# Kernel tuning notes

Measured on AMD Instinct MI355X. Metric: run time of the kernel, lower is better.

Reference implementation:

```python
import jax, jax.numpy as jnp
import numpy as np

B, S, HIDDEN, NH = 2, 2048, 1024, 16
D = HIDDEN // NH  # 64
PHYS_W, CONS_W = 0.2, 0.15
LN_EPS = 1e-5


def _layernorm(x, gamma, beta):
    mu = jnp.mean(x, axis=-1, keepdims=True)
    var = jnp.mean(jnp.square(x - mu), axis=-1, keepdims=True)
    return (x - mu) * jax.lax.rsqrt(var + LN_EPS) * gamma + beta


def setup_inputs() -> dict:
    key = jax.random.key(0)
    ks = jax.random.split(key, 12)
    s = 0.02
    return {
        "cnn_features": jax.random.normal(ks[0], (B, S, HIDDEN), jnp.float32),
        "llm_features": jax.random.normal(ks[1], (B, S, HIDDEN), jnp.float32),
        # Linear weights stored [in, out] so y = x @ W + b (torch's W.T)
        "Wq": jax.random.normal(ks[2], (HIDDEN, HIDDEN), jnp.float32) * s,
        "bq": jnp.zeros((HIDDEN,), jnp.float32),
        "Wk": jax.random.normal(ks[3], (HIDDEN, HIDDEN), jnp.float32) * s,
        "bk": jnp.zeros((HIDDEN,), jnp.float32),
        "Wv": jax.random.normal(ks[4], (HIDDEN, HIDDEN), jnp.float32) * s,
        "bv": jnp.zeros((HIDDEN,), jnp.float32),
        "Wo": jax.random.normal(ks[5], (HIDDEN, HIDDEN), jnp.float32) * s,
        "bo": jnp.zeros((HIDDEN,), jnp.float32),
        "energy_emb": jax.random.normal(ks[6], (1, 1, HIDDEN), jnp.float32),
        "mass_emb": jax.random.normal(ks[7], (1, 1, HIDDEN), jnp.float32),
        "momentum_emb": jax.random.normal(ks[8], (1, 1, HIDDEN), jnp.float32),
        "gamma": jnp.ones((HIDDEN,), jnp.float32),
        "beta": jnp.zeros((HIDDEN,), jnp.float32),
    }


def reference(cnn_features, llm_features, Wq, bq, Wk, bk, Wv, bv, Wo, bo,
              energy_emb, mass_emb, momentum_emb, gamma, beta):
    Bsz, Sc, _ = cnn_features.shape
    Sl = llm_features.shape[1]

    def attn(q_in, kv_in):
        Sq, Sk = q_in.shape[1], kv_in.shape[1]
        Q = (q_in @ Wq + bq).reshape(Bsz, Sq, NH, D).transpose(0, 2, 1, 3)   # bhqd
        K = (kv_in @ Wk + bk).reshape(Bsz, Sk, NH, D).transpose(0, 2, 1, 3)  # bhkd
        V = (kv_in @ Wv + bv).reshape(Bsz, Sk, NH, D).transpose(0, 2, 1, 3)  # bhkd
        scores = jnp.einsum('bhqd,bhkd->bhqk', Q, K) / np.float32(np.sqrt(D))
        # physics biases: require Sq == Sk (elementwise Q*K), shape [B,H,Sq,1]
        energy_bias = jnp.sum(Q * K, axis=-1, keepdims=True) * PHYS_W
        mass_bias = jnp.mean(Q + K, axis=-1, keepdims=True) * CONS_W
        attn_w = jax.nn.softmax(scores + energy_bias + mass_bias, axis=-1)
        attended = jnp.einsum('bhqk,bhkd->bhqd', attn_w, V)
        attended = attended.transpose(0, 2, 1, 3).reshape(Bsz, Sq, HIDDEN)
        out = attended @ Wo + bo
        return _layernorm(q_in + out, gamma, beta)

    phys = jnp.concatenate([
        jnp.broadcast_to(energy_emb, (Bsz, 1, HIDDEN)),
        jnp.broadcast_to(mass_emb, (Bsz, 1, HIDDEN)),
        jnp.broadcast_to(momentum_emb, (Bsz, 1, HIDDEN)),
    ], axis=1)  # [B, 3, HIDDEN]
    aug_cnn = jnp.concatenate([cnn_features, phys], axis=1)  # [B, Sc+3, H]
    aug_llm = jnp.concatenate([llm_features, phys], axis=1)  # [B, Sl+3, H]

    cnn_att = attn(aug_cnn, aug_llm)
    llm_att = attn(aug_llm, aug_cnn)
    return cnn_att[:, :Sc, :], llm_att[:, :Sl, :]
```

## Files before the change

### kernel.cpp

```cpp
#include <hip/hip_runtime.h>

#define BN 2
#define SS 2048
#define SA 2051
#define HID 1024
#define NHD 16
#define DH 64
#define GSTR 32
#define VTLD 8320
#define KSTR 72
#define VSTR 40
#define MFMA16 __builtin_amdgcn_mfma_f32_16x16x32_bf16
#define QSCALE 0.18033688011112042f

typedef __attribute__((ext_vector_type(4))) float floatx4;
typedef __attribute__((ext_vector_type(8))) short bf16x8;
typedef __attribute__((ext_vector_type(2))) unsigned uintx2;

__device__ __forceinline__ float bf2f(short s) {
  union { unsigned u; float f; } v; v.u = ((unsigned)(unsigned short)s) << 16; return v.f;
}
__device__ __forceinline__ short f2bf(float f) {
  union { float f; unsigned u; } v; v.f = f;
  unsigned u = v.u;
  u += 0x7FFF + ((u >> 16) & 1);
  return (short)(u >> 16);
}
__device__ __forceinline__ unsigned pack2(float lo, float hi) {
  unsigned ul = __float_as_uint(lo) + 0x8000u;
  unsigned uh = __float_as_uint(hi) + 0x8000u;
  return __builtin_amdgcn_perm(uh, ul, 0x07060302u);
}
__device__ __forceinline__ unsigned cvtpk(float lo, float hi) {
  unsigned r;
  asm("v_cvt_pk_bf16_f32 %0, %1, %2" : "=v"(r) : "v"(lo), "v"(hi));
  return r;
}
__device__ __forceinline__ float exp2fast(float x) {
#if __has_builtin(__builtin_amdgcn_exp2f)
  return __builtin_amdgcn_exp2f(x);
#else
  float r; asm("v_exp_f32 %0, %1" : "=v"(r) : "v"(x)); return r;
#endif
}
__device__ __forceinline__ uintx2 qtrans(unsigned A, unsigned B) {
  auto t = __builtin_amdgcn_permlane32_swap(A, B, false, false);
  auto u = __builtin_amdgcn_permlane16_swap(t[0], t[1], false, false);
  uintx2 r; r[0] = u[0]; r[1] = u[1];
  return r;
}
__device__ __forceinline__ void gload16(const short* g, short* l) {
  __builtin_amdgcn_global_load_lds(
      (const __attribute__((address_space(1))) void*)g,
      (__attribute__((address_space(3))) void*)l, 16, 0, 0);
}
__device__ __forceinline__ bool in_is_f32(const unsigned* graw) {
  return graw[0] == 0x3F800000u;
}

__global__ __launch_bounds__(256) void convert_in(const void* __restrict__ src, long off,
                                                  short* __restrict__ dst, int n,
                                                  const unsigned* __restrict__ graw) {
  bool f32 = in_is_f32(graw);
  int i = (blockIdx.x * 256 + threadIdx.x) * 4;
  int stride = gridDim.x * 1024;
  if (f32) {
    const float* s = (const float*)src + off;
    for (; i < n; i += stride) {
      float4 v = *(const float4*)(s + i);
      short4 o; o.x = f2bf(v.x); o.y = f2bf(v.y); o.z = f2bf(v.z); o.w = f2bf(v.w);
      *(short4*)(dst + i) = o;
    }
  } else {
    const short* s = (const short*)src + off;
    for (; i < n; i += stride)
      *(short4*)(dst + i) = *(const short4*)(s + i);
  }
}

__global__ __launch_bounds__(256) void convert_small(
    const void* s0, const void* s1, const void* s2, const void* s3,
    const void* s4, const void* s5, const void* s6, const void* s7,
    const void* s8, short* __restrict__ dst, const unsigned* __restrict__ graw) {
  bool f32 = in_is_f32(graw);
  const void* srcs[9] = {s0, s1, s2, s3, s4, s5, s6, s7, s8};
  const void* s = srcs[blockIdx.x];
  short* d = dst + (size_t)blockIdx.x * 1024;
  for (int i = threadIdx.x; i < 1024; i += 256)
    d[i] = f32 ? f2bf(((const float*)s)[i]) : ((const short*)s)[i];
}

__global__ __launch_bounds__(256) void conv_wt(const void* __restrict__ W,
    short* __restrict__ WT, const unsigned* __restrict__ graw) {
  __shared__ short tile[32][33];
  bool f32 = in_is_f32(graw);
  int n0 = blockIdx.x * 32, k0 = blockIdx.y * 32;
  int tx = threadIdx.x & 31, ty = threadIdx.x >> 5;
#pragma unroll
  for (int i = 0; i < 4; i++) {
    int k = k0 + ty + i*8;
    short v = f32 ? f2bf(((const float*)W)[(size_t)k * HID + n0 + tx])
                  : ((const short*)W)[(size_t)k * HID + n0 + tx];
    tile[ty + i*8][tx] = v;
  }
  __syncthreads();
#pragma unroll
  for (int i = 0; i < 4; i++)
    WT[(size_t)(n0 + ty + i*8) * HID + k0 + tx] = tile[tx][ty + i*8];
}

__global__ __launch_bounds__(256) void gemm_bf(
    const short* __restrict__ A, int tailA,
    const short* __restrict__ B, int tailB,
    const short* __restrict__ embB,
    const short* __restrict__ bias, int bias_row, float scale,
    short* __restrict__ out16, float* __restrict__ out32, long ldc,
    const void* __restrict__ rc0, const void* __restrict__ rc1,
    const unsigned* __restrict__ graw) {
  __shared__ __align__(16) short sA[128 * GSTR];
  __shared__ __align__(16) short sB[128 * GSTR];
  int t = threadIdx.x;
  int wave = t >> 6, lane = t & 63, l16 = lane & 15, quad = lane >> 4;
  int nwg = gridDim.x * gridDim.y;
  int bid = blockIdx.y * gridDim.x + blockIdx.x;
  int cpx = nwg >> 3;
  int swz = (bid & 7) * cpx + (bid >> 3);
  int bx = swz % gridDim.x, by = swz / gridDim.x;
  int m0 = by * 128, n0 = bx * 128;
  int msub = (wave >> 1) * 64, nsub = (wave & 1) * 64;

  const short* apr[2]; const short* bpr[2]; short* ldA[2]; short* ldB[2];
#pragma unroll
  for (int rep = 0; rep < 2; rep++) {
    int cid = rep * 256 + t;
    int row = cid >> 2, kc = (cid & 3) * 8;
    int ra = m0 + row;
    const short* ap;
    if (tailA && ra >= 8192) ap = embB + (size_t)((ra > 8194 ? 8194 : ra) - 8192) * 1024;
    else                     ap = A + (size_t)ra * HID;
    int rb = n0 + row;
    const short* bp;
    if (tailB && rb >= 8192) bp = embB + (size_t)((rb > 8194 ? 8194 : rb) - 8192) * 1024;
    else                     bp = B + (size_t)rb * HID;
    apr[rep] = ap + kc; bpr[rep] = bp + kc;
    ldA[rep] = &sA[(rep*256 + wave*64) * 8];
    ldB[rep] = &sB[(rep*256 + wave*64) * 8];
  }
#pragma unroll
  for (int rep = 0; rep < 2; rep++) {
    gload16(apr[rep], ldA[rep]);
    gload16(bpr[rep], ldB[rep]);
  }

  floatx4 acc[4][4] = {};
  for (int k0 = 0; k0 < HID; k0 += 32) {
    __syncthreads();
    bf16x8 af[4], bf_[4];
#pragma unroll
    for (int i = 0; i < 4; i++) {
      af[i]  = *(const bf16x8*)(&sA[(msub + i*16 + l16) * GSTR + quad*8]);
      bf_[i] = *(const bf16x8*)(&sB[(nsub + i*16 + l16) * GSTR + quad*8]);
    }
    __syncthreads();
    if (k0 + 32 < HID) {
#pragma unroll
      for (int rep = 0; rep < 2; rep++) {
        gload16(apr[rep] + k0 + 32, ldA[rep]);
        gload16(bpr[rep] + k0 + 32, ldB[rep]);
      }
    }
#pragma unroll
    for (int mi = 0; mi < 4; mi++)
#pragma unroll
      for (int ni = 0; ni < 4; ni++)
        acc[mi][ni] = MFMA16(af[mi], bf_[ni], acc[mi][ni], 0, 0, 0);
  }

  bool f32in = in_is_f32(graw);
#pragma unroll
  for (int mi = 0; mi < 4; mi++)
#pragma unroll
    for (int ni = 0; ni < 4; ni++) {
      int col = n0 + nsub + ni*16 + l16;
      float bcol = bias_row ? 0.f : bf2f(bias[col]);
#pragma unroll
      for (int r = 0; r < 4; r++) {
        int m = m0 + msub + mi*16 + quad*4 + r;
        float v = (acc[mi][ni][r] + (bias_row ? bf2f(bias[m]) : bcol)) * scale;
        if (out32) {
          float res;
          if (f32in) res = ((const float*)(m < 4096 ? rc0 : rc1))[(size_t)(m & 4095) * HID + col];
          else       res = bf2f(((const short*)(m < 4096 ? rc0 : rc1))[(size_t)(m & 4095) * HID + col]);
          out32[(size_t)m * HID + col] = v + res;
        } else {
          out16[(size_t)m * ldc + col] = f2bf(v);
        }
      }
    }
}

__global__ __launch_bounds__(256, 4) void flash3(
    const short* __restrict__ Qa, const short* __restrict__ Ka,
    const short* __restrict__ VTa, short* __restrict__ att) {
  __shared__ __align__(16) short sK0[32*KSTR], sK1[32*KSTR];
  __shared__ __align__(16) short sV0[64*VSTR], sV1[64*VSTR];
  int t = threadIdx.x, wave = t >> 6, lane = t & 63;
  int l16 = lane & 15, quad = lane >> 4;
  int bid = blockIdx.x;
  int swz = (bid & 7) * 128 + (bid >> 3);
  int qt  = swz & 15;
  int h   = (swz >> 4) & 15;
  int sb  = swz >> 8;
  int side = sb >> 1, b = sb & 1;
  int qrow0 = side * 4096 + b * 2048;
  int kvb = (side ^ 1) * 4096 + b * 2048;
  int q0 = qt * 128 + wave * 32;

  const short* qp0 = Qa + (size_t)(qrow0 + q0 + l16) * HID + h*DH + quad*8;
  const short* qp1 = qp0 + 16 * HID;
  bf16x8 qa0 = *(const bf16x8*)qp0, qb0 = *(const bf16x8*)(qp0 + 32);
  bf16x8 qa1 = *(const bf16x8*)qp1, qb1 = *(const bf16x8*)(qp1 + 32);

  float rs0 = 0.f, rs1 = 0.f;
  floatx4 oA[4] = {}, oB[4] = {};

  int krow = t >> 3, kc8 = (t & 7) * 8;
  int vrow = t >> 2, vc8 = (t & 3) * 8;
  const short* kgp = Ka + (size_t)(kvb + krow) * HID + h*DH + kc8;
  const short* vgp = VTa + (size_t)(h*DH + vrow) * VTLD + kvb + vc8;
  bf16x8 kreg = *(const bf16x8*)kgp;
  bf16x8 vreg = *(const bf16x8*)vgp;
  short *kw = sK0, *vw = sV0, *ka = sK1, *va = sV1;

  for (int kv0 = 0; kv0 < 2048; kv0 += 32) {
    *(bf16x8*)(kw + krow*KSTR + kc8) = kreg;
    *(bf16x8*)(vw + vrow*VSTR + vc8) = vreg;
    __syncthreads();
    kgp += 32*HID; vgp += 32;
    kreg = *(const bf16x8*)kgp;
    vreg = *(const bf16x8*)vgp;

    bf16x8 k00 = *(const bf16x8*)(kw + l16*KSTR + quad*8);
    bf16x8 k01 = *(const bf16x8*)(kw + l16*KSTR + 32 + quad*8);
    bf16x8 k10 = *(const bf16x8*)(kw + (16 + l16)*KSTR + quad*8);
    bf16x8 k11 = *(const bf16x8*)(kw + (16 + l16)*KSTR + 32 + quad*8);
    bf16x8 v0 = *(const bf16x8*)(vw + l16*VSTR + quad*8);
    bf16x8 v1 = *(const bf16x8*)(vw + (16 + l16)*VSTR + quad*8);
    bf16x8 v2 = *(const bf16x8*)(vw + (32 + l16)*VSTR + quad*8);
    bf16x8 v3 = *(const bf16x8*)(vw + (48 + l16)*VSTR + quad*8);

    floatx4 s00 = {}, s10 = {}, s01 = {}, s11 = {};
    __builtin_amdgcn_s_setprio(1);
    s00 = MFMA16(k00, qa0, s00, 0, 0, 0); s00 = MFMA16(k01, qb0, s00, 0, 0, 0);
    s10 = MFMA16(k10, qa0, s10, 0, 0, 0); s10 = MFMA16(k11, qb0, s10, 0, 0, 0);
    s01 = MFMA16(k00, qa1, s01, 0, 0, 0); s01 = MFMA16(k01, qb1, s01, 0, 0, 0);
    s11 = MFMA16(k10, qa1, s11, 0, 0, 0); s11 = MFMA16(k11, qb1, s11, 0, 0, 0);
    __builtin_amdgcn_s_setprio(0);

    floatx4 p00, p10, p01, p11;
#pragma unroll
    for (int r = 0; r < 4; r++) {
      p00[r] = exp2fast(s00[r]); p10[r] = exp2fast(s10[r]);
      p01[r] = exp2fast(s01[r]); p11[r] = exp2fast(s11[r]);
    }
    rs0 += ((p00[0]+p00[1])+(p00[2]+p00[3])) + ((p10[0]+p10[1])+(p10[2]+p10[3]));
    rs1 += ((p01[0]+p01[1])+(p01[2]+p01[3])) + ((p11[0]+p11[1])+(p11[2]+p11[3]));

    unsigned pc00 = cvtpk(p00[0], p00[1]), pc01 = cvtpk(p00[2], p00[3]);
    unsigned pc10 = cvtpk(p10[0], p10[1]), pc11 = cvtpk(p10[2], p10[3]);
    unsigned pd00 = cvtpk(p01[0], p01[1]), pd01 = cvtpk(p01[2], p01[3]);
    unsigned pd10 = cvtpk(p11[0], p11[1]), pd11 = cvtpk(p11[2], p11[3]);
    uintx2 uA0 = qtrans(pc00, pc10);
    uintx2 uA1 = qtrans(pc01, pc11);
    uintx2 uB0 = qtrans(pd00, pd10);
    uintx2 uB1 = qtrans(pd01, pd11);
    union { unsigned u[4]; bf16x8 v; } pf0, pf1;
    pf0.u[0] = uA0[0]; pf0.u[1] = uA1[0]; pf0.u[2] = uA0[1]; pf0.u[3] = uA1[1];
    pf1.u[0] = uB0[0]; pf1.u[1] = uB1[0]; pf1.u[2] = uB0[1]; pf1.u[3] = uB1[1];

    __builtin_amdgcn_s_setprio(1);
    oA[0] = MFMA16(v0, pf0.v, oA[0], 0, 0, 0);
    oA[1] = MFMA16(v1, pf0.v, oA[1], 0, 0, 0);
    oA[2] = MFMA16(v2, pf0.v, oA[2], 0, 0, 0);
    oA[3] = MFMA16(v3, pf0.v, oA[3], 0, 0, 0);
    oB[0] = MFMA16(v0, pf1.v, oB[0], 0, 0, 0);
    oB[1] = MFMA16(v1, pf1.v, oB[1], 0, 0, 0);
    oB[2] = MFMA16(v2, pf1.v, oB[2], 0, 0, 0);
    oB[3] = MFMA16(v3, pf1.v, oB[3], 0, 0, 0);
    __builtin_amdgcn_s_setprio(0);

    short* tk = kw; kw = ka; ka = tk;
    short* tv = vw; vw = va; va = tv;
  }

  {
    int er = l16 < 2 ? l16 : 2;
    const short* kpt = Ka + (size_t)(8192 + er) * HID + h*DH + quad*8;
    bf16x8 tk0 = *(const bf16x8*)kpt;
    bf16x8 tk1 = *(const bf16x8*)(kpt + 32);
    floatx4 s00 = {}, s01 = {};
    s00 = MFMA16(tk0, qa0, s00, 0, 0, 0); s00 = MFMA16(tk1, qb0, s00, 0, 0, 0);
    s01 = MFMA16(tk0, qa1, s01, 0, 0, 0); s01 = MFMA16(tk1, qb1, s01, 0, 0, 0);
    floatx4 p00, p01;
#pragma unroll
    for (int r = 0; r < 4; r++) {
      bool val = (quad == 0) && (r < 3);
      p00[r] = val ? exp2fast(s00[r]) : 0.f;
      p01[r] = val ? exp2fast(s01[r]) : 0.f;
    }
    rs0 += (p00[0]+p00[1]) + (p00[2]+p00[3]);
    rs1 += (p01[0]+p01[1]) + (p01[2]+p01[3]);
    unsigned pc00 = cvtpk(p00[0], p00[1]), pc01 = cvtpk(p00[2], p00[3]);
    unsigned pd00 = cvtpk(p01[0], p01[1]), pd01 = cvtpk(p01[2], p01[3]);
    uintx2 uA0 = qtrans(pc00, 0u);
    uintx2 uA1 = qtrans(pc01, 0u);
    uintx2 uB0 = qtrans(pd00, 0u);
    uintx2 uB1 = qtrans(pd01, 0u);
    union { unsigned u[4]; bf16x8 v; } pf0, pf1;
    pf0.u[0] = uA0[0]; pf0.u[1] = uA1[0]; pf0.u[2] = uA0[1]; pf0.u[3] = uA1[1];
    pf1.u[0] = uB0[0]; pf1.u[1] = uB1[0]; pf1.u[2] = uB0[1]; pf1.u[3] = uB1[1];
    const short* vtp = VTa + (size_t)(h*DH + l16) * VTLD + 8192 + quad*8;
    bf16x8 v0 = *(const bf16x8*)vtp;
    bf16x8 v1 = *(const bf16x8*)(vtp + 16*VTLD);
    bf16x8 v2 = *(const bf16x8*)(vtp + 32*VTLD);
    bf16x8 v3 = *(const bf16x8*)(vtp + 48*VTLD);
    oA[0] = MFMA16(v0, pf0.v, oA[0], 0, 0, 0);
    oA[1] = MFMA16(v1, pf0.v, oA[1], 0, 0, 0);
    oA[2] = MFMA16(v2, pf0.v, oA[2], 0, 0, 0);
    oA[3] = MFMA16(v3, pf0.v, oA[3], 0, 0, 0);
    oB[0] = MFMA16(v0, pf1.v, oB[0], 0, 0, 0);
    oB[1] = MFMA16(v1, pf1.v, oB[1], 0, 0, 0);
    oB[2] = MFMA16(v2, pf1.v, oB[2], 0, 0, 0);
    oB[3] = MFMA16(v3, pf1.v, oB[3], 0, 0, 0);
  }

  rs0 += __shfl_xor(rs0, 16, 64); rs0 += __shfl_xor(rs0, 32, 64);
  rs1 += __shfl_xor(rs1, 16, 64); rs1 += __shfl_xor(rs1, 32, 64);
  float i0 = 1.f / rs0, i1 = 1.f / rs1;

  unsigned* ob0 = (unsigned*)(att + (size_t)(qrow0 + q0 + l16) * HID + h*DH + quad*4);
  unsigned* ob1 = (unsigned*)(att + (size_t)(qrow0 + q0 + 16 + l16) * HID + h*DH + quad*4);
#pragma unroll
  for (int n = 0; n < 4; n++) {
    ob0[n*8]     = pack2(oA[n][0]*i0, oA[n][1]*i0);
    ob0[n*8 + 1] = pack2(oA[n][2]*i0, oA[n][3]*i0);
    ob1[n*8]     = pack2(oB[n][0]*i1, oB[n][1]*i1);
    ob1[n*8 + 1] = pack2(oB[n][2]*i1, oB[n][3]*i1);
  }
}

__global__ __launch_bounds__(256) void ln_kernel(
    const float* __restrict__ y, const short* __restrict__ gamma,
    const short* __restrict__ beta, void* __restrict__ outp, long orow,
    const unsigned* __restrict__ graw) {
  bool f32o = in_is_f32(graw);
  int row = blockIdx.x;
  int t = threadIdx.x;
  const float* yr = y + (size_t)row * HID;
  float4 v = ((const float4*)yr)[t];
  float sum = v.x + v.y + v.z + v.w;
#pragma unroll
  for (int off = 32; off >= 1; off >>= 1) sum += __shfl_xor(sum, off, 64);
  __shared__ float red[8];
  int wave = t >> 6, lane = t & 63;
  if (lane == 0) red[wave] = sum;
  __syncthreads();
  float mu = (red[0] + red[1] + red[2] + red[3]) * (1.f/HID);
  float dx = v.x - mu, dy = v.y - mu, dz = v.z - mu, dw = v.w - mu;
  float sq = dx*dx + dy*dy + dz*dz + dw*dw;
#pragma unroll
  for (int off = 32; off >= 1; off >>= 1) sq += __shfl_xor(sq, off, 64);
  if (lane == 0) red[4 + wave] = sq;
  __syncthreads();
  float var = (red[4] + red[5] + red[6] + red[7]) * (1.f/HID);
  float inv = rsqrtf(var + 1e-5f);
  const short* g = gamma + t*4;
  const short* be = beta + t*4;
  float o0 = dx * inv * bf2f(g[0]) + bf2f(be[0]);
  float o1 = dy * inv * bf2f(g[1]) + bf2f(be[1]);
  float o2 = dz * inv * bf2f(g[2]) + bf2f(be[2]);
  float o3 = dw * inv * bf2f(g[3]) + bf2f(be[3]);
  size_t base = (size_t)(orow + row) * HID + t*4;
  if (f32o) {
    float4 ov = {o0, o1, o2, o3};
    *(float4*)((float*)outp + base) = ov;
  } else {
    short4 ov = {f2bf(o0), f2bf(o1), f2bf(o2), f2bf(o3)};
    *(short4*)((short*)outp + base) = ov;
  }
}

extern "C" void kernel_launch(void* const* d_in, const int* in_sizes, int n_in,
                              void* d_out, int out_size, void* d_ws, size_t ws_size,
                              hipStream_t stream) {
  const void* cnn = d_in[0];
  const void* llm = d_in[1];
  const void* Wq  = d_in[2];
  const void* bq  = d_in[3];
  const void* Wk  = d_in[4];
  const void* bk  = d_in[5];
  const void* Wv  = d_in[6];
  const void* bv  = d_in[7];
  const void* Wo  = d_in[8];
  const void* bo  = d_in[9];
  const void* ee  = d_in[10];
  const void* me  = d_in[11];
  const void* pe  = d_in[12];
  const void* gamma = d_in[13];
  const void* beta  = d_in[14];
  const unsigned* graw = (const unsigned*)gamma;
  (void)in_sizes; (void)n_in; (void)out_size; (void)ws_size;

  char* p = (char*)d_ws;
  auto alloc = [&](size_t bytes) { char* r = p; p += (bytes + 255) & ~(size_t)255; return r; };
  short* WqT = (short*)alloc((size_t)HID*HID*2);
  short* WkT = (short*)alloc((size_t)HID*HID*2);
  short* WvT = (short*)alloc((size_t)HID*HID*2);
  short* WoT = (short*)alloc((size_t)HID*HID*2);
  short* smallB = (short*)alloc(9 * 1024 * 2);
  short* Qa  = (short*)alloc((size_t)8192 * HID * 2);
  short* Ka  = (short*)alloc((size_t)8320 * HID * 2);
  short* VT  = (short*)alloc((size_t)HID * VTLD * 2);
  float* y   = (float*)Qa;
  short* att = (short*)d_out;
  short* Xa  = (short*)d_out + (size_t)8192 * HID;
  short* bqB = smallB;        short* bkB = smallB + 1024;
  short* bvB = smallB + 2048; short* boB = smallB + 3072;
  short* embB = smallB + 4096;
  short* gB  = smallB + 7168; short* bB  = smallB + 8192;

  dim3 tb(256);
  dim3 tg(32, 32);
  const int NF = 4096 * HID;

  convert_in<<<dim3(NF/1024), tb, 0, stream>>>(cnn, 0, Xa, NF, graw);
  convert_in<<<dim3(NF/1024), tb, 0, stream>>>(llm, 0, Xa + (size_t)NF, NF, graw);
  conv_wt<<<tg, tb, 0, stream>>>(Wq, WqT, graw);
  conv_wt<<<tg, tb, 0, stream>>>(Wk, WkT, graw);
  conv_wt<<<tg, tb, 0, stream>>>(Wv, WvT, graw);
  conv_wt<<<tg, tb, 0, stream>>>(Wo, WoT, graw);
  convert_small<<<dim3(9), tb, 0, stream>>>(bq, bk, bv, bo, ee, me, pe, gamma, beta,
                                            smallB, graw);

  gemm_bf<<<dim3(8, 64), tb, 0, stream>>>(Xa, 0, WqT, 0, embB, bqB, 0, QSCALE,
      Qa, nullptr, HID, cnn, llm, graw);
  gemm_bf<<<dim3(8, 65), tb, 0, stream>>>(Xa, 1, WkT, 0, embB, bkB, 0, 1.f,
      Ka, nullptr, HID, cnn, llm, graw);
  gemm_bf<<<dim3(65, 8), tb, 0, stream>>>(WvT, 0, Xa, 1, embB, bvB, 1, 1.f,
      VT, nullptr, VTLD, cnn, llm, graw);

  flash3<<<dim3(1024), tb, 0, stream>>>(Qa, Ka, VT, att);

  gemm_bf<<<dim3(8, 64), tb, 0, stream>>>(att, 0, WoT, 0, embB, boB, 0, 1.f,
      nullptr, y, HID, cnn, llm, graw);

  ln_kernel<<<dim3(8192), tb, 0, stream>>>(y, gB, bB, d_out, 0, graw);
}
```

Baseline: 384.8 us.

## Double-buffer GEMM LDS, merge QKV projections into one launch, shrink flash tiles

The GEMM core now uses two LDS buffers. The next K-slice loads while MFMAs run on the current one, which cuts the per-iteration syncs from two to one. The three Q/K/V projection GEMMs are merged into a single launch with a swizzled block index that picks each block's role. The attention kernel now gives each wave 16 query rows instead of 32, doubles the grid to 2048 blocks and raises launch bounds to 8 blocks per CU for more occupancy. The trade-off is that every K/V tile loaded into LDS is reused by half as many queries.

```diff
diff --git a/kernel.cpp b/kernel.cpp
--- a/kernel.cpp
+++ b/kernel.cpp
@@ -6,7 +6,6 @@
 #define HID 1024
 #define NHD 16
 #define DH 64
-#define GSTR 32
 #define VTLD 8320
 #define KSTR 72
 #define VSTR 40
@@ -109,27 +108,74 @@
     WT[(size_t)(n0 + ty + i*8) * HID + k0 + tx] = tile[tx][ty + i*8];
 }
 
-__global__ __launch_bounds__(256) void gemm_bf(
-    const short* __restrict__ A, int tailA,
-    const short* __restrict__ B, int tailB,
-    const short* __restrict__ embB,
-    const short* __restrict__ bias, int bias_row, float scale,
-    short* __restrict__ out16, float* __restrict__ out32, long ldc,
-    const void* __restrict__ rc0, const void* __restrict__ rc1,
-    const unsigned* __restrict__ graw) {
-  __shared__ __align__(16) short sA[128 * GSTR];
-  __shared__ __align__(16) short sB[128 * GSTR];
+__device__ __forceinline__ void gemm_core_2ph(
+    const short* apr0, const short* apr1,
+    const short* bpr0, const short* bpr1,
+    short* sA, short* sB, int wave, int l16, int quad, int msub, int nsub,
+    floatx4 acc[4][4]) {
+  gload16(apr0, sA + wave*512);  gload16(apr1, sA + 2048 + wave*512);
+  gload16(bpr0, sB + wave*512);  gload16(bpr1, sB + 2048 + wave*512);
+  __syncthreads();
+  int cur = 0;
+  for (int k0 = 0; k0 < HID; k0 += 32) {
+    if (k0 + 32 < HID) {
+      int nx = cur ^ 1;
+      gload16(apr0 + k0 + 32, sA + nx*4096 + wave*512);
+      gload16(apr1 + k0 + 32, sA + nx*4096 + 2048 + wave*512);
+      gload16(bpr0 + k0 + 32, sB + nx*4096 + wave*512);
+      gload16(bpr1 + k0 + 32, sB + nx*4096 + 2048 + wave*512);
+    }
+    const short* cA = sA + cur*4096;
+    const short* cB = sB + cur*4096;
+    bf16x8 af[4], bf_[4];
+#pragma unroll
+    for (int i = 0; i < 4; i++) {
+      af[i]  = *(const bf16x8*)(cA + (msub + i*16 + l16)*32 + quad*8);
+      bf_[i] = *(const bf16x8*)(cB + (nsub + i*16 + l16)*32 + quad*8);
+    }
+#pragma unroll
+    for (int mi = 0; mi < 4; mi++)
+#pragma unroll
+      for (int ni = 0; ni < 4; ni++)
+        acc[mi][ni] = MFMA16(af[mi], bf_[ni], acc[mi][ni], 0, 0, 0);
+    __syncthreads();
+    cur ^= 1;
+  }
+}
+
+__global__ __launch_bounds__(256) void gemm_qkv(
+    const short* __restrict__ Xa, const short* __restrict__ WqT,
+    const short* __restrict__ WkT, const short* __restrict__ WvT,
+    const short* __restrict__ embB, const short* __restrict__ bqB,
+    const short* __restrict__ bkB, const short* __restrict__ bvB,
+    short* __restrict__ Qa, short* __restrict__ Ka, short* __restrict__ VT) {
+  __shared__ __align__(16) short sA[2*4096];
+  __shared__ __align__(16) short sB[2*4096];
   int t = threadIdx.x;
   int wave = t >> 6, lane = t & 63, l16 = lane & 15, quad = lane >> 4;
-  int nwg = gridDim.x * gridDim.y;
-  int bid = blockIdx.y * gridDim.x + blockIdx.x;
-  int cpx = nwg >> 3;
-  int swz = (bid & 7) * cpx + (bid >> 3);
-  int bx = swz % gridDim.x, by = swz / gridDim.x;
-  int m0 = by * 128, n0 = bx * 128;
+  int bid = blockIdx.x;
+  int swz = (bid & 7) * 194 + (bid >> 3);
+
+  const short *A, *B, *bias; short* out; long ldc;
+  int m0, n0, tailA, tailB, bias_row; float scale;
+  if (swz < 512) {
+    A = Xa; B = WqT; bias = bqB; out = Qa; ldc = HID;
+    m0 = (swz >> 3) * 128; n0 = (swz & 7) * 128;
+    tailA = 0; tailB = 0; bias_row = 0; scale = QSCALE;
+  } else if (swz < 1032) {
+    int id = swz - 512;
+    A = Xa; B = WkT; bias = bkB; out = Ka; ldc = HID;
+    m0 = (id >> 3) * 128; n0 = (id & 7) * 128;
+    tailA = 1; tailB = 0; bias_row = 0; scale = 1.f;
+  } else {
+    int id = swz - 1032;
+    A = WvT; B = Xa; bias = bvB; out = VT; ldc = VTLD;
+    m0 = (id / 65) * 128; n0 = (id % 65) * 128;
+    tailA = 0; tailB = 1; bias_row = 1; scale = 1.f;
+  }
   int msub = (wave >> 1) * 64, nsub = (wave & 1) * 64;
 
-  const short* apr[2]; const short* bpr[2]; short* ldA[2]; short* ldB[2];
+  const short* apr[2]; const short* bpr[2];
 #pragma unroll
   for (int rep = 0; rep < 2; rep++) {
     int cid = rep * 256 + t;
@@ -143,40 +189,12 @@
     if (tailB && rb >= 8192) bp = embB + (size_t)((rb > 8194 ? 8194 : rb) - 8192) * 1024;
     else                     bp = B + (size_t)rb * HID;
     apr[rep] = ap + kc; bpr[rep] = bp + kc;
-    ldA[rep] = &sA[(rep*256 + wave*64) * 8];
-    ldB[rep] = &sB[(rep*256 + wave*64) * 8];
-  }
-#pragma unroll
-  for (int rep = 0; rep < 2; rep++) {
-    gload16(apr[rep], ldA[rep]);
-    gload16(bpr[rep], ldB[rep]);
   }
 
   floatx4 acc[4][4] = {};
-  for (int k0 = 0; k0 < HID; k0 += 32) {
-    __syncthreads();
-    bf16x8 af[4], bf_[4];
-#pragma unroll
-    for (int i = 0; i < 4; i++) {
-      af[i]  = *(const bf16x8*)(&sA[(msub + i*16 + l16) * GSTR + quad*8]);
-      bf_[i] = *(const bf16x8*)(&sB[(nsub + i*16 + l16) * GSTR + quad*8]);
-    }
-    __syncthreads();
-    if (k0 + 32 < HID) {
-#pragma unroll
-      for (int rep = 0; rep < 2; rep++) {
-        gload16(apr[rep] + k0 + 32, ldA[rep]);
-        gload16(bpr[rep] + k0 + 32, ldB[rep]);
-      }
-    }
-#pragma unroll
-    for (int mi = 0; mi < 4; mi++)
-#pragma unroll
-      for (int ni = 0; ni < 4; ni++)
-        acc[mi][ni] = MFMA16(af[mi], bf_[ni], acc[mi][ni], 0, 0, 0);
-  }
-
-  bool f32in = in_is_f32(graw);
+  gemm_core_2ph(apr[0], apr[1], bpr[0], bpr[1], sA, sB,
+                wave, l16, quad, msub, nsub, acc);
+
 #pragma unroll
   for (int mi = 0; mi < 4; mi++)
 #pragma unroll
@@ -187,19 +205,62 @@
       for (int r = 0; r < 4; r++) {
         int m = m0 + msub + mi*16 + quad*4 + r;
         float v = (acc[mi][ni][r] + (bias_row ? bf2f(bias[m]) : bcol)) * scale;
-        if (out32) {
-          float res;
-          if (f32in) res = ((const float*)(m < 4096 ? rc0 : rc1))[(size_t)(m & 4095) * HID + col];
-          else       res = bf2f(((const short*)(m < 4096 ? rc0 : rc1))[(size_t)(m & 4095) * HID + col]);
-          out32[(size_t)m * HID + col] = v + res;
-        } else {
-          out16[(size_t)m * ldc + col] = f2bf(v);
-        }
+        out[(size_t)m * ldc + col] = f2bf(v);
       }
     }
 }
 
-__global__ __launch_bounds__(256, 4) void flash3(
+__global__ __launch_bounds__(256) void gemm_bf(
+    const short* __restrict__ A, const short* __restrict__ B,
+    const short* __restrict__ bias, float scale,
+    float* __restrict__ out32,
+    const void* __restrict__ rc0, const void* __restrict__ rc1,
+    const unsigned* __restrict__ graw) {
+  __shared__ __align__(16) short sA[2*4096];
+  __shared__ __align__(16) short sB[2*4096];
+  int t = threadIdx.x;
+  int wave = t >> 6, lane = t & 63, l16 = lane & 15, quad = lane >> 4;
+  int nwg = gridDim.x * gridDim.y;
+  int bid = blockIdx.y * gridDim.x + blockIdx.x;
+  int cpx = nwg >> 3;
+  int swz = (bid & 7) * cpx + (bid >> 3);
+  int bx = swz % gridDim.x, by = swz / gridDim.x;
+  int m0 = by * 128, n0 = bx * 128;
+  int msub = (wave >> 1) * 64, nsub = (wave & 1) * 64;
+
+  const short* apr[2]; const short* bpr[2];
+#pragma unroll
+  for (int rep = 0; rep < 2; rep++) {
+    int cid = rep * 256 + t;
+    int row = cid >> 2, kc = (cid & 3) * 8;
+    apr[rep] = A + (size_t)(m0 + row) * HID + kc;
+    bpr[rep] = B + (size_t)(n0 + row) * HID + kc;
+  }
+
+  floatx4 acc[4][4] = {};
+  gemm_core_2ph(apr[0], apr[1], bpr[0], bpr[1], sA, sB,
+                wave, l16, quad, msub, nsub, acc);
+
+  bool f32in = in_is_f32(graw);
+#pragma unroll
+  for (int mi = 0; mi < 4; mi++)
+#pragma unroll
+    for (int ni = 0; ni < 4; ni++) {
+      int col = n0 + nsub + ni*16 + l16;
+      float bcol = bf2f(bias[col]);
+#pragma unroll
+      for (int r = 0; r < 4; r++) {
+        int m = m0 + msub + mi*16 + quad*4 + r;
+        float v = (acc[mi][ni][r] + bcol) * scale;
+        float res;
+        if (f32in) res = ((const float*)(m < 4096 ? rc0 : rc1))[(size_t)(m & 4095) * HID + col];
+        else       res = bf2f(((const short*)(m < 4096 ? rc0 : rc1))[(size_t)(m & 4095) * HID + col]);
+        out32[(size_t)m * HID + col] = v + res;
+      }
+    }
+}
+
+__global__ __launch_bounds__(256, 8) void flash3(
     const short* __restrict__ Qa, const short* __restrict__ Ka,
     const short* __restrict__ VTa, short* __restrict__ att) {
   __shared__ __align__(16) short sK0[32*KSTR], sK1[32*KSTR];
@@ -207,22 +268,20 @@
   int t = threadIdx.x, wave = t >> 6, lane = t & 63;
   int l16 = lane & 15, quad = lane >> 4;
   int bid = blockIdx.x;
-  int swz = (bid & 7) * 128 + (bid >> 3);
-  int qt  = swz & 15;
-  int h   = (swz >> 4) & 15;
-  int sb  = swz >> 8;
+  int swz = (bid & 7) * 256 + (bid >> 3);
+  int qt  = swz & 31;
+  int h   = (swz >> 5) & 15;
+  int sb  = swz >> 9;
   int side = sb >> 1, b = sb & 1;
   int qrow0 = side * 4096 + b * 2048;
   int kvb = (side ^ 1) * 4096 + b * 2048;
-  int q0 = qt * 128 + wave * 32;
+  int q0 = qt * 64 + wave * 16;
 
   const short* qp0 = Qa + (size_t)(qrow0 + q0 + l16) * HID + h*DH + quad*8;
-  const short* qp1 = qp0 + 16 * HID;
   bf16x8 qa0 = *(const bf16x8*)qp0, qb0 = *(const bf16x8*)(qp0 + 32);
-  bf16x8 qa1 = *(const bf16x8*)qp1, qb1 = *(const bf16x8*)(qp1 + 32);
-
-  float rs0 = 0.f, rs1 = 0.f;
-  floatx4 oA[4] = {}, oB[4] = {};
+
+  float rs0 = 0.f;
+  floatx4 oA[4] = {};
 
   int krow = t >> 3, kc8 = (t & 7) * 8;
   int vrow = t >> 2, vc8 = (t & 3) * 8;
@@ -249,44 +308,31 @@
     bf16x8 v2 = *(const bf16x8*)(vw + (32 + l16)*VSTR + quad*8);
     bf16x8 v3 = *(const bf16x8*)(vw + (48 + l16)*VSTR + quad*8);
 
-    floatx4 s00 = {}, s10 = {}, s01 = {}, s11 = {};
+    floatx4 s00 = {}, s10 = {};
     __builtin_amdgcn_s_setprio(1);
     s00 = MFMA16(k00, qa0, s00, 0, 0, 0); s00 = MFMA16(k01, qb0, s00, 0, 0, 0);
     s10 = MFMA16(k10, qa0, s10, 0, 0, 0); s10 = MFMA16(k11, qb0, s10, 0, 0, 0);
-    s01 = MFMA16(k00, qa1, s01, 0, 0, 0); s01 = MFMA16(k01, qb1, s01, 0, 0, 0);
-    s11 = MFMA16(k10, qa1, s11, 0, 0, 0); s11 = MFMA16(k11, qb1, s11, 0, 0, 0);
     __builtin_amdgcn_s_setprio(0);
 
-    floatx4 p00, p10, p01, p11;
+    floatx4 p00, p10;
 #pragma unroll
     for (int r = 0; r < 4; r++) {
       p00[r] = exp2fast(s00[r]); p10[r] = exp2fast(s10[r]);
-      p01[r] = exp2fast(s01[r]); p11[r] = exp2fast(s11[r]);
     }
     rs0 += ((p00[0]+p00[1])+(p00[2]+p00[3])) + ((p10[0]+p10[1])+(p10[2]+p10[3]));
-    rs1 += ((p01[0]+p01[1])+(p01[2]+p01[3])) + ((p11[0]+p11[1])+(p11[2]+p11[3]));
 
     unsigned pc00 = cvtpk(p00[0], p00[1]), pc01 = cvtpk(p00[2], p00[3]);
     unsigned pc10 = cvtpk(p10[0], p10[1]), pc11 = cvtpk(p10[2], p10[3]);
-    unsigned pd00 = cvtpk(p01[0], p01[1]), pd01 = cvtpk(p01[2], p01[3]);
-    unsigned pd10 = cvtpk(p11[0], p11[1]), pd11 = cvtpk(p11[2], p11[3]);
     uintx2 uA0 = qtrans(pc00, pc10);
     uintx2 uA1 = qtrans(pc01, pc11);
-    uintx2 uB0 = qtrans(pd00, pd10);
-    uintx2 uB1 = qtrans(pd01, pd11);
-    union { unsigned u[4]; bf16x8 v; } pf0, pf1;
+    union { unsigned u[4]; bf16x8 v; } pf0;
     pf0.u[0] = uA0[0]; pf0.u[1] = uA1[0]; pf0.u[2] = uA0[1]; pf0.u[3] = uA1[1];
-    pf1.u[0] = uB0[0]; pf1.u[1] = uB1[0]; pf1.u[2] = uB0[1]; pf1.u[3] = uB1[1];
 
     __builtin_amdgcn_s_setprio(1);
     oA[0] = MFMA16(v0, pf0.v, oA[0], 0, 0, 0);
     oA[1] = MFMA16(v1, pf0.v, oA[1], 0, 0, 0);
     oA[2] = MFMA16(v2, pf0.v, oA[2], 0, 0, 0);
     oA[3] = MFMA16(v3, pf0.v, oA[3], 0, 0, 0);
-    oB[0] = MFMA16(v0, pf1.v, oB[0], 0, 0, 0);
-    oB[1] = MFMA16(v1, pf1.v, oB[1], 0, 0, 0);
-    oB[2] = MFMA16(v2, pf1.v, oB[2], 0, 0, 0);
-    oB[3] = MFMA16(v3, pf1.v, oB[3], 0, 0, 0);
     __builtin_amdgcn_s_setprio(0);
 
     short* tk = kw; kw = ka; ka = tk;
@@ -298,27 +344,20 @@
     const short* kpt = Ka + (size_t)(8192 + er) * HID + h*DH + quad*8;
     bf16x8 tk0 = *(const bf16x8*)kpt;
     bf16x8 tk1 = *(const bf16x8*)(kpt + 32);
-    floatx4 s00 = {}, s01 = {};
+    floatx4 s00 = {};
     s00 = MFMA16(tk0, qa0, s00, 0, 0, 0); s00 = MFMA16(tk1, qb0, s00, 0, 0, 0);
-    s01 = MFMA16(tk0, qa1, s01, 0, 0, 0); s01 = MFMA16(tk1, qb1, s01, 0, 0, 0);
-    floatx4 p00, p01;
+    floatx4 p00;
 #pragma unroll
     for (int r = 0; r < 4; r++) {
       bool val = (quad == 0) && (r < 3);
       p00[r] = val ? exp2fast(s00[r]) : 0.f;
-      p01[r] = val ? exp2fast(s01[r]) : 0.f;
     }
     rs0 += (p00[0]+p00[1]) + (p00[2]+p00[3]);
-    rs1 += (p01[0]+p01[1]) + (p01[2]+p01[3]);
     unsigned pc00 = cvtpk(p00[0], p00[1]), pc01 = cvtpk(p00[2], p00[3]);
-    unsigned pd00 = cvtpk(p01[0], p01[1]), pd01 = cvtpk(p01[2], p01[3]);
     uintx2 uA0 = qtrans(pc00, 0u);
     uintx2 uA1 = qtrans(pc01, 0u);
-    uintx2 uB0 = qtrans(pd00, 0u);
-    uintx2 uB1 = qtrans(pd01, 0u);
-    union { unsigned u[4]; bf16x8 v; } pf0, pf1;
+    union { unsigned u[4]; bf16x8 v; } pf0;
     pf0.u[0] = uA0[0]; pf0.u[1] = uA1[0]; pf0.u[2] = uA0[1]; pf0.u[3] = uA1[1];
-    pf1.u[0] = uB0[0]; pf1.u[1] = uB1[0]; pf1.u[2] = uB0[1]; pf1.u[3] = uB1[1];
     const short* vtp = VTa + (size_t)(h*DH + l16) * VTLD + 8192 + quad*8;
     bf16x8 v0 = *(const bf16x8*)vtp;
     bf16x8 v1 = *(const bf16x8*)(vtp + 16*VTLD);
@@ -328,24 +367,16 @@
     oA[1] = MFMA16(v1, pf0.v, oA[1], 0, 0, 0);
     oA[2] = MFMA16(v2, pf0.v, oA[2], 0, 0, 0);
     oA[3] = MFMA16(v3, pf0.v, oA[3], 0, 0, 0);
-    oB[0] = MFMA16(v0, pf1.v, oB[0], 0, 0, 0);
-    oB[1] = MFMA16(v1, pf1.v, oB[1], 0, 0, 0);
-    oB[2] = MFMA16(v2, pf1.v, oB[2], 0, 0, 0);
-    oB[3] = MFMA16(v3, pf1.v, oB[3], 0, 0, 0);
   }
 
   rs0 += __shfl_xor(rs0, 16, 64); rs0 += __shfl_xor(rs0, 32, 64);
-  rs1 += __shfl_xor(rs1, 16, 64); rs1 += __shfl_xor(rs1, 32, 64);
-  float i0 = 1.f / rs0, i1 = 1.f / rs1;
+  float i0 = 1.f / rs0;
 
   unsigned* ob0 = (unsigned*)(att + (size_t)(qrow0 + q0 + l16) * HID + h*DH + quad*4);
-  unsigned* ob1 = (unsigned*)(att + (size_t)(qrow0 + q0 + 16 + l16) * HID + h*DH + quad*4);
 #pragma unroll
   for (int n = 0; n < 4; n++) {
     ob0[n*8]     = pack2(oA[n][0]*i0, oA[n][1]*i0);
     ob0[n*8 + 1] = pack2(oA[n][2]*i0, oA[n][3]*i0);
-    ob1[n*8]     = pack2(oB[n][0]*i1, oB[n][1]*i1);
-    ob1[n*8 + 1] = pack2(oB[n][2]*i1, oB[n][3]*i1);
   }
 }
 
@@ -442,17 +473,12 @@
   convert_small<<<dim3(9), tb, 0, stream>>>(bq, bk, bv, bo, ee, me, pe, gamma, beta,
                                             smallB, graw);
 
-  gemm_bf<<<dim3(8, 64), tb, 0, stream>>>(Xa, 0, WqT, 0, embB, bqB, 0, QSCALE,
-      Qa, nullptr, HID, cnn, llm, graw);
-  gemm_bf<<<dim3(8, 65), tb, 0, stream>>>(Xa, 1, WkT, 0, embB, bkB, 0, 1.f,
-      Ka, nullptr, HID, cnn, llm, graw);
-  gemm_bf<<<dim3(65, 8), tb, 0, stream>>>(WvT, 0, Xa, 1, embB, bvB, 1, 1.f,
-      VT, nullptr, VTLD, cnn, llm, graw);
-
-  flash3<<<dim3(1024), tb, 0, stream>>>(Qa, Ka, VT, att);
-
-  gemm_bf<<<dim3(8, 64), tb, 0, stream>>>(att, 0, WoT, 0, embB, boB, 0, 1.f,
-      nullptr, y, HID, cnn, llm, graw);
+  gemm_qkv<<<dim3(1552), tb, 0, stream>>>(Xa, WqT, WkT, WvT, embB,
+                                          bqB, bkB, bvB, Qa, Ka, VT);
+
+  flash3<<<dim3(2048), tb, 0, stream>>>(Qa, Ka, VT, att);
+
+  gemm_bf<<<dim3(8, 64), tb, 0, stream>>>(att, WoT, boB, 1.f, y, cnn, llm, graw);
 
   ln_kernel<<<dim3(8192), tb, 0, stream>>>(y, gB, bB, d_out, 0, graw);
 }
```

Result: slower. 634.4 us (+64.9%).
